# Kernel tuning notes

Hardware: AMD Instinct MI355X
Metric: run time of the kernel (lower is better)

## Reference

```python
import jax, jax.numpy as jnp
import numpy as np

B, S, D_MODEL, N_HEADS, D_K, D_V = 4, 2048, 512, 8, 64, 64
LN_EPS = 1e-5


def setup_inputs() -> dict:
    key = jax.random.key(0)
    ks = jax.random.split(key, 8)
    inp = {
        "input_Q": jax.random.normal(ks[0], (B, S, D_MODEL), dtype=jnp.float32),
        "input_K": jax.random.normal(ks[1], (B, S, D_MODEL), dtype=jnp.float32),
        "input_V": jax.random.normal(ks[2], (B, S, D_MODEL), dtype=jnp.float32),
        "attn_mask": jax.random.randint(ks[3], (B, S, S), 0, 2).astype(jnp.bool_),
        # weights stored [in, out] (torch Linear does x @ W.T; here we use x @ W)
        "W_Q": jax.random.normal(ks[4], (D_MODEL, N_HEADS * D_K), dtype=jnp.float32) * 0.02,
        "W_K": jax.random.normal(ks[5], (D_MODEL, N_HEADS * D_K), dtype=jnp.float32) * 0.02,
        "W_V": jax.random.normal(ks[6], (D_MODEL, N_HEADS * D_V), dtype=jnp.float32) * 0.02,
        "W_O": jax.random.normal(ks[7], (N_HEADS * D_V, D_MODEL), dtype=jnp.float32) * 0.02,
    }
    return inp


def _layernorm(x, eps=LN_EPS):
    mu = jnp.mean(x, axis=-1, keepdims=True)
    var = jnp.mean(jnp.square(x - mu), axis=-1, keepdims=True)
    return (x - mu) * jax.lax.rsqrt(var + eps)


def reference(input_Q, input_K, input_V, attn_mask, W_Q, W_K, W_V, W_O):
    b = input_Q.shape[0]
    # project and split heads: [b, h, s, d]
    Q = (input_Q @ W_Q).reshape(b, -1, N_HEADS, D_K).transpose(0, 2, 1, 3)
    K = (input_K @ W_K).reshape(b, -1, N_HEADS, D_K).transpose(0, 2, 1, 3)
    V = (input_V @ W_V).reshape(b, -1, N_HEADS, D_V).transpose(0, 2, 1, 3)
    scale = 1.0 / np.sqrt(D_K).astype(np.float32)
    # [b, h, s_q, s_k] scores, mask broadcast over heads
    scores = jnp.einsum("bhqd,bhkd->bhqk", Q, K) * scale
    scores = jnp.where(attn_mask[:, None, :, :], jnp.float32(-1e9), scores)
    attn = jax.nn.softmax(scores, axis=-1)
    context = jnp.einsum("bhqk,bhkd->bhqd", attn, V)
    context = context.transpose(0, 2, 1, 3).reshape(b, -1, N_HEADS * D_V)
    output = context @ W_O
    out = _layernorm(output + input_Q)
    return out, attn
```

## Files before the change

kernel.cpp:

```cpp
#include <hip/hip_runtime.h>
#include <hip/hip_bf16.h>
#include <stdint.h>

#define B_  4
#define S_  2048
#define DM  512
#define H_  8
#define DK  64

typedef float        f32x4 __attribute__((ext_vector_type(4)));
typedef short        s16x8 __attribute__((ext_vector_type(8)));
typedef short        s16x4 __attribute__((ext_vector_type(4)));
typedef unsigned int u32x4 __attribute__((ext_vector_type(4)));
typedef unsigned long long u64x4 __attribute__((ext_vector_type(4)));

#define MFMA_B16(a,b,c) __builtin_amdgcn_mfma_f32_16x16x32_bf16(a,b,c,0,0,0)

__device__ __forceinline__ uint32_t bfr(float x) {
  uint32_t u = __float_as_uint(x);
  return (u + 0x7fffu + ((u >> 16) & 1u)) >> 16;
}
__device__ __forceinline__ uint32_t pk2(float a, float b) {
  return ((bfr(b) & 0xffffu) << 16) | (bfr(a) & 0xffffu);
}
__device__ __forceinline__ float uf16(short s) {
  return __uint_as_float(((uint32_t)(uint16_t)s) << 16);
}

__global__ __launch_bounds__(256) void wt_k(const float* __restrict__ w0,
                                            const float* __restrict__ w1,
                                            const float* __restrict__ w2,
                                            const float* __restrict__ w3,
                                            uint16_t* __restrict__ Wt) {
  __shared__ float Ls[64 * 65];
  const int tid = threadIdx.x;
  const int z = blockIdx.z;
  const float* W = (z == 0) ? w0 : (z == 1) ? w1 : (z == 2) ? w2 : w3;
  const int k0 = blockIdx.x * 64, n0 = blockIdx.y * 64;
  {
    const int r = tid >> 2, c = (tid & 3) * 16;
    const float4* src = (const float4*)(W + (size_t)(k0 + r) * 512 + n0 + c);
    float4 v0 = src[0], v1 = src[1], v2 = src[2], v3 = src[3];
    float* d = Ls + r * 65 + c;
    d[0]=v0.x; d[1]=v0.y; d[2]=v0.z;  d[3]=v0.w;
    d[4]=v1.x; d[5]=v1.y; d[6]=v1.z;  d[7]=v1.w;
    d[8]=v2.x; d[9]=v2.y; d[10]=v2.z; d[11]=v2.w;
    d[12]=v3.x;d[13]=v3.y;d[14]=v3.z; d[15]=v3.w;
  }
  __syncthreads();
  uint16_t* dstbase = Wt + (size_t)z * 262144;
#pragma unroll
  for (int i = 0; i < 2; ++i) {
    int nl = i * 32 + (tid >> 3);
    int kc = (tid & 7) * 8;
    s16x8 v;
#pragma unroll
    for (int jj = 0; jj < 8; ++jj) v[jj] = (short)bfr(Ls[(kc + jj) * 65 + nl]);
    *(s16x8*)(dstbase + (size_t)(n0 + nl) * 512 + k0 + kc) = v;
  }
}

__global__ __launch_bounds__(256) void maskpack_k(const int* __restrict__ mask,
                                                  unsigned long long* __restrict__ mbits) {
  const int lane = threadIdx.x & 63;
  const int wid = (blockIdx.x * 256 + threadIdx.x) >> 6;
  for (int w0 = wid * 4; w0 < B_ * S_ * 32; w0 += 8192 * 4) {
    int v0 = __builtin_nontemporal_load(mask + (size_t)(w0 + 0) * 64 + lane);
    int v1 = __builtin_nontemporal_load(mask + (size_t)(w0 + 1) * 64 + lane);
    int v2 = __builtin_nontemporal_load(mask + (size_t)(w0 + 2) * 64 + lane);
    int v3 = __builtin_nontemporal_load(mask + (size_t)(w0 + 3) * 64 + lane);
    unsigned long long b0 = __ballot(v0 != 0), b1 = __ballot(v1 != 0);
    unsigned long long b2 = __ballot(v2 != 0), b3 = __ballot(v3 != 0);
    if (lane == 0) { u64x4 t = {b0, b1, b2, b3}; *(u64x4*)(mbits + w0) = t; }
  }
}

template <bool PROJ>
__global__ __launch_bounds__(256) void gemm2_k(const float* __restrict__ Xq,
                                               const float* __restrict__ Xk,
                                               const float* __restrict__ Xv,
                                               const uint16_t* __restrict__ Wt,
                                               const uint16_t* __restrict__ Actx,
                                               uint16_t* __restrict__ Qkv,
                                               float* __restrict__ Y) {
  __shared__ __hip_bfloat16 As[64 * 64];
  __shared__ __hip_bfloat16 Bs[64 * 64];
  const int tid = threadIdx.x, lane = tid & 63, w = tid >> 6;
  const int l4 = lane >> 4, lc = lane & 15;
  const int p = blockIdx.x;
  const int L = PROJ ? ((p & 7) * 384 + (p >> 3)) : ((p & 7) * 128 + (p >> 3));
  const int yn = L & 7;
  const int xm = PROJ ? ((L >> 3) & 127) : (L >> 3);
  const int z  = PROJ ? (L >> 10) : 3;
  const int m0 = xm * 64, n0 = yn * 64;
  const float* Af = PROJ ? ((z == 0) ? Xq : (z == 1) ? Xk : Xv) : nullptr;
  const uint16_t* Bt = Wt + (size_t)z * 262144;
  const int wm = (w >> 1) * 32, wn = (w & 1) * 32;
  const int ar = tid >> 2, ac = (tid & 3) * 16;
  f32x4 acc[2][2] = {};

  float4 ra[4]; s16x8 rab[2]; s16x8 rb[2];
  auto loadA = [&](int kk) {
    if constexpr (PROJ) {
      const float4* s = (const float4*)(Af + (size_t)(m0 + ar) * 512 + kk + ac);
      ra[0] = s[0]; ra[1] = s[1]; ra[2] = s[2]; ra[3] = s[3];
    } else {
      const uint16_t* s = Actx + (size_t)(m0 + ar) * 512 + kk + ac;
      rab[0] = *(const s16x8*)s; rab[1] = *(const s16x8*)(s + 8);
    }
  };
  auto loadB = [&](int kk) {
    const uint16_t* s = Bt + (size_t)(n0 + ar) * 512 + kk + ac;
    rb[0] = *(const s16x8*)s; rb[1] = *(const s16x8*)(s + 8);
  };
  auto writeAB = [&]() {
    char* da = (char*)As + ar * 128;
    char* db = (char*)Bs + ar * 128;
    const int c0 = (ac * 2) ^ ((ar & 7) << 4);
    const int c1 = (ac * 2 + 16) ^ ((ar & 7) << 4);
    if constexpr (PROJ) {
      u32x4 p0, p1;
      p0.x = pk2(ra[0].x, ra[0].y); p0.y = pk2(ra[0].z, ra[0].w);
      p0.z = pk2(ra[1].x, ra[1].y); p0.w = pk2(ra[1].z, ra[1].w);
      p1.x = pk2(ra[2].x, ra[2].y); p1.y = pk2(ra[2].z, ra[2].w);
      p1.z = pk2(ra[3].x, ra[3].y); p1.w = pk2(ra[3].z, ra[3].w);
      *(u32x4*)(da + c0) = p0; *(u32x4*)(da + c1) = p1;
    } else {
      *(s16x8*)(da + c0) = rab[0]; *(s16x8*)(da + c1) = rab[1];
    }
    *(s16x8*)(db + c0) = rb[0]; *(s16x8*)(db + c1) = rb[1];
  };

  loadA(0); loadB(0); writeAB();
  __syncthreads();
  for (int t = 0; t < 8; ++t) {
    if (t < 7) { loadA((t + 1) * 64); loadB((t + 1) * 64); }
    s16x8 af[2], bg[2];
    __builtin_amdgcn_s_setprio(1);
#pragma unroll
    for (int kf = 0; kf < 2; ++kf) {
#pragma unroll
      for (int mf = 0; mf < 2; ++mf) {
        int row = wm + mf * 16 + lc;
        af[mf] = *(const s16x8*)((char*)As + row * 128 +
                                 ((kf * 64 + l4 * 16) ^ ((row & 7) << 4)));
      }
#pragma unroll
      for (int nf = 0; nf < 2; ++nf) {
        int row = wn + nf * 16 + lc;
        bg[nf] = *(const s16x8*)((char*)Bs + row * 128 +
                                 ((kf * 64 + l4 * 16) ^ ((row & 7) << 4)));
      }
#pragma unroll
      for (int mf = 0; mf < 2; ++mf)
#pragma unroll
        for (int nf = 0; nf < 2; ++nf)
          acc[mf][nf] = MFMA_B16(af[mf], bg[nf], acc[mf][nf]);
    }
    __builtin_amdgcn_s_setprio(0);
    if (t < 7) {
      __syncthreads();
      writeAB();
      __syncthreads();
    }
  }
#pragma unroll
  for (int mf = 0; mf < 2; ++mf)
#pragma unroll
    for (int nf = 0; nf < 2; ++nf) {
      int row = m0 + wm + mf * 16 + l4 * 4;
      int col = n0 + wn + nf * 16 + lc;
#pragma unroll
      for (int j = 0; j < 4; ++j) {
        if constexpr (PROJ)
          (Qkv + (size_t)z * 4194304)[(size_t)(row + j) * 512 + col] =
              (uint16_t)bfr(acc[mf][nf][j]);
        else
          Y[(size_t)(row + j) * 512 + col] = acc[mf][nf][j];
      }
    }
}

__global__ __launch_bounds__(256) void attn_k(const uint16_t* __restrict__ Qb,
                                              const uint16_t* __restrict__ Kb,
                                              const uint16_t* __restrict__ Vb,
                                              const unsigned long long* __restrict__ mbits,
                                              float* __restrict__ attn_out,
                                              uint16_t* __restrict__ ctx) {
  __shared__ __hip_bfloat16 Ks[2][64 * 64];
  __shared__ __hip_bfloat16 Vt[64 * 64];
  __shared__ __hip_bfloat16 Ps[4][16 * 72];
  const int tid = threadIdx.x, lane = tid & 63, w = tid >> 6;
  const int l4 = lane >> 4, lc = lane & 15;
  const int p = blockIdx.x;
  const int L = (p & 7) * 128 + (p >> 3);
  const int qt = L & 31, h = (L >> 5) & 7, b = L >> 8;
  const int qbase = qt * 64;
  const int srow = tid >> 3, scol = tid & 7;

  s16x8 aq0, aq1;
  {
    const uint16_t* qp = Qb + ((size_t)(b * S_ + qbase + w * 16 + lc)) * DM + h * DK + l4 * 8;
    aq0 = *(const s16x8*)qp;
    aq1 = *(const s16x8*)(qp + 32);
  }
  const uint16_t* Kbase = Kb + (size_t)(b * S_) * DM + h * DK;
  const uint16_t* Vbase = Vb + (size_t)(b * S_) * DM + h * DK;
  const unsigned long long* mrow = mbits + ((size_t)(b * S_) + qbase + w * 16 + l4 * 4) * 32;

  float lrun[4] = {0.f, 0.f, 0.f, 0.f};
#pragma unroll
  for (int i = 0; i < 2; ++i) {
    int row = i * 32 + srow;
    s16x8 v = *(const s16x8*)(Kbase + (size_t)row * DM + scol * 8);
    *(s16x8*)((char*)Ks[0] + row * 128 + ((scol * 16) ^ ((row & 7) << 4))) = v;
  }
  __syncthreads();
  for (int kt = 0; kt < 32; ++kt) {
    const int cur = kt & 1;
    const int nxt = (kt < 31) ? kt + 1 : kt;
    s16x8 rk0 = *(const s16x8*)(Kbase + (size_t)(nxt * 64 + srow) * DM + scol * 8);
    s16x8 rk1 = *(const s16x8*)(Kbase + (size_t)(nxt * 64 + 32 + srow) * DM + scol * 8);
    unsigned long long mws[4];
#pragma unroll
    for (int j = 0; j < 4; ++j) mws[j] = mrow[j * 32 + kt];
    f32x4 sacc[4] = {};
    __builtin_amdgcn_s_setprio(1);
#pragma unroll
    for (int nf = 0; nf < 4; ++nf) {
      int row = nf * 16 + lc;
#pragma unroll
      for (int kf = 0; kf < 2; ++kf) {
        s16x8 bk = *(const s16x8*)((char*)Ks[cur] + row * 128 +
                                   ((kf * 64 + l4 * 16) ^ ((row & 7) << 4)));
        sacc[nf] = MFMA_B16(kf ? aq1 : aq0, bk, sacc[nf]);
      }
    }
    __builtin_amdgcn_s_setprio(0);
#pragma unroll
    for (int j = 0; j < 4; ++j)
#pragma unroll
      for (int nf = 0; nf < 4; ++nf) {
        float e = __expf(sacc[nf][j] * 0.125f);
        lrun[j] += ((mws[j] >> (nf * 16 + lc)) & 1ull) ? 0.f : e;
      }
    *(s16x8*)((char*)Ks[cur ^ 1] + srow * 128 + ((scol * 16) ^ ((srow & 7) << 4))) = rk0;
    {
      int row = 32 + srow;
      *(s16x8*)((char*)Ks[cur ^ 1] + row * 128 + ((scol * 16) ^ ((row & 7) << 4))) = rk1;
    }
    __syncthreads();
  }
#pragma unroll
  for (int off = 1; off < 16; off <<= 1)
#pragma unroll
    for (int j = 0; j < 4; ++j) lrun[j] += __shfl_xor(lrun[j], off);
  float Li[4];
#pragma unroll
  for (int j = 0; j < 4; ++j) Li[j] = 1.f / lrun[j];

#pragma unroll
  for (int i = 0; i < 2; ++i) {
    int row = i * 32 + srow;
    s16x8 v = *(const s16x8*)(Kbase + (size_t)row * DM + scol * 8);
    *(s16x8*)((char*)Ks[0] + row * 128 + ((scol * 16) ^ ((row & 7) << 4))) = v;
    s16x8 vv = *(const s16x8*)(Vbase + (size_t)row * DM + scol * 8);
#pragma unroll
    for (int jj = 0; jj < 8; ++jj) {
      int d = scol * 8 + jj;
      *(int16_t*)((char*)Vt + ((d * 128 + row * 2) ^ (scol << 4))) = vv[jj];
    }
  }
  __syncthreads();
  f32x4 cacc[4] = {};
  float* arow = attn_out + (((size_t)(b * H_ + h)) * S_ + qbase + w * 16) * S_;
  for (int kt = 0; kt < 32; ++kt) {
    const int cur = kt & 1;
    const int nxt = (kt < 31) ? kt + 1 : kt;
    s16x8 rk0 = *(const s16x8*)(Kbase + (size_t)(nxt * 64 + srow) * DM + scol * 8);
    s16x8 rk1 = *(const s16x8*)(Kbase + (size_t)(nxt * 64 + 32 + srow) * DM + scol * 8);
    s16x8 rv0 = *(const s16x8*)(Vbase + (size_t)(nxt * 64 + srow) * DM + scol * 8);
    s16x8 rv1 = *(const s16x8*)(Vbase + (size_t)(nxt * 64 + 32 + srow) * DM + scol * 8);
    unsigned long long mws[4];
#pragma unroll
    for (int j = 0; j < 4; ++j) mws[j] = mrow[j * 32 + kt];
    f32x4 sacc[4] = {};
    __builtin_amdgcn_s_setprio(1);
#pragma unroll
    for (int nf = 0; nf < 4; ++nf) {
      int row = nf * 16 + lc;
#pragma unroll
      for (int kf = 0; kf < 2; ++kf) {
        s16x8 bk = *(const s16x8*)((char*)Ks[cur] + row * 128 +
                                   ((kf * 64 + l4 * 16) ^ ((row & 7) << 4)));
        sacc[nf] = MFMA_B16(kf ? aq1 : aq0, bk, sacc[nf]);
      }
    }
    __builtin_amdgcn_s_setprio(0);
#pragma unroll
    for (int j = 0; j < 4; ++j)
#pragma unroll
      for (int nf = 0; nf < 4; ++nf) {
        float e = __expf(sacc[nf][j] * 0.125f);
        float p2 = ((mws[j] >> (nf * 16 + lc)) & 1ull) ? 0.f : e * Li[j];
        *(uint16_t*)((char*)Ps[w] + (l4 * 4 + j) * 144 + (nf * 16 + lc) * 2) = (uint16_t)bfr(p2);
      }
    s16x8 ap0 = *(const s16x8*)((char*)Ps[w] + lc * 144 + l4 * 16);
    s16x8 ap1 = *(const s16x8*)((char*)Ps[w] + lc * 144 + 64 + l4 * 16);
#pragma unroll
    for (int j = 0; j < 4; ++j) {
      const int r = j * 4 + (lane >> 4);
      s16x4 pv = *(const s16x4*)((char*)Ps[w] + r * 144 + (lane & 15) * 8);
      f32x4 o;
      o[0] = uf16(pv[0]); o[1] = uf16(pv[1]); o[2] = uf16(pv[2]); o[3] = uf16(pv[3]);
      __builtin_nontemporal_store(o,
          (f32x4*)(arow + (size_t)r * S_ + kt * 64 + (lane & 15) * 4));
    }
    __builtin_amdgcn_s_setprio(1);
#pragma unroll
    for (int nf = 0; nf < 4; ++nf) {
      int d = nf * 16 + lc;
#pragma unroll
      for (int kf = 0; kf < 2; ++kf) {
        s16x8 bv = *(const s16x8*)((char*)Vt +
                     ((d * 128 + kf * 64 + l4 * 16) ^ ((((d >> 3)) & 7) << 4)));
        cacc[nf] = MFMA_B16(kf ? ap1 : ap0, bv, cacc[nf]);
      }
    }
    __builtin_amdgcn_s_setprio(0);
    __syncthreads();
    *(s16x8*)((char*)Ks[cur ^ 1] + srow * 128 + ((scol * 16) ^ ((srow & 7) << 4))) = rk0;
    {
      int row = 32 + srow;
      *(s16x8*)((char*)Ks[cur ^ 1] + row * 128 + ((scol * 16) ^ ((row & 7) << 4))) = rk1;
    }
#pragma unroll
    for (int jj = 0; jj < 8; ++jj) {
      int d = scol * 8 + jj;
      *(int16_t*)((char*)Vt + ((d * 128 + srow * 2) ^ (scol << 4))) = rv0[jj];
      *(int16_t*)((char*)Vt + ((d * 128 + (32 + srow) * 2) ^ (scol << 4))) = rv1[jj];
    }
    __syncthreads();
  }
#pragma unroll
  for (int nf = 0; nf < 4; ++nf) {
    int d = nf * 16 + lc;
#pragma unroll
    for (int j = 0; j < 4; ++j) {
      int q = qbase + w * 16 + l4 * 4 + j;
      ctx[((size_t)(b * S_ + q)) * DM + h * DK + d] = (uint16_t)bfr(cacc[nf][j]);
    }
  }
}

__global__ __launch_bounds__(256) void ln_k(const float* __restrict__ Y,
                                            const float* __restrict__ X,
                                            float* __restrict__ out) {
  const int lane = threadIdx.x & 63, w = threadIdx.x >> 6;
  const size_t row = (size_t)blockIdx.x * 4 + w;
  const float4* y = (const float4*)(Y + row * 512);
  const float4* x = (const float4*)(X + row * 512);
  float4 a0 = y[lane * 2], a1 = y[lane * 2 + 1];
  float4 b0 = x[lane * 2], b1 = x[lane * 2 + 1];
  float v[8] = {a0.x + b0.x, a0.y + b0.y, a0.z + b0.z, a0.w + b0.w,
                a1.x + b1.x, a1.y + b1.y, a1.z + b1.z, a1.w + b1.w};
  float s = 0.f, ss = 0.f;
#pragma unroll
  for (int j = 0; j < 8; ++j) { s += v[j]; ss += v[j] * v[j]; }
#pragma unroll
  for (int off = 1; off < 64; off <<= 1) {
    s += __shfl_xor(s, off);
    ss += __shfl_xor(ss, off);
  }
  float mean = s * (1.f / 512.f);
  float var = ss * (1.f / 512.f) - mean * mean;
  float rstd = rsqrtf(var + 1e-5f);
  float4 o0 = make_float4((v[0] - mean) * rstd, (v[1] - mean) * rstd,
                          (v[2] - mean) * rstd, (v[3] - mean) * rstd);
  float4 o1 = make_float4((v[4] - mean) * rstd, (v[5] - mean) * rstd,
                          (v[6] - mean) * rstd, (v[7] - mean) * rstd);
  float4* o = (float4*)(out + row * 512);
  o[lane * 2] = o0;
  o[lane * 2 + 1] = o1;
}

extern "C" void kernel_launch(void* const* d_in, const int* in_sizes, int n_in,
                              void* d_out, int out_size, void* d_ws, size_t ws_size,
                              hipStream_t stream) {
  const float* Xq = (const float*)d_in[0];
  const float* Xk = (const float*)d_in[1];
  const float* Xv = (const float*)d_in[2];
  const int*   mask = (const int*)d_in[3];
  const float* Wq = (const float*)d_in[4];
  const float* Wk = (const float*)d_in[5];
  const float* Wv = (const float*)d_in[6];
  const float* Wo = (const float*)d_in[7];

  float* out  = (float*)d_out;
  float* attn = out + (size_t)B_ * S_ * DM;

  char* ws = (char*)d_ws;
  uint16_t* Qb = (uint16_t*)(ws);
  uint16_t* Kb = (uint16_t*)(ws + (8u  << 20));
  uint16_t* Vb = (uint16_t*)(ws + (16u << 20));
  uint16_t* Cx = (uint16_t*)(ws + (24u << 20));
  float*    Y  = (float*)   (ws + (32u << 20));
  uint16_t* Wt = (uint16_t*)(ws + (48u << 20));
  unsigned long long* mb = (unsigned long long*)(ws + (50u << 20));

  wt_k<<<dim3(8, 8, 4), 256, 0, stream>>>(Wq, Wk, Wv, Wo, Wt);
  maskpack_k<<<2048, 256, 0, stream>>>(mask, mb);

  gemm2_k<true><<<3072, 256, 0, stream>>>(Xq, Xk, Xv, Wt, nullptr, Qb, nullptr);

  attn_k<<<1024, 256, 0, stream>>>(Qb, Kb, Vb, mb, attn, Cx);

  gemm2_k<false><<<1024, 256, 0, stream>>>(nullptr, nullptr, nullptr, Wt, Cx, nullptr, Y);
  ln_k<<<2048, 256, 0, stream>>>(Y, Xq, out);
}
```

Baseline: 238.5 us.

## Enlarge GEMM tiles to 128x128 and merge weight-transpose with mask packing

The projection and output GEMMs now use 128x128 block tiles, with each wave computing a 64x64 sub-tile (4x4 MFMA fragments) instead of 32x32. This raises data reuse per LDS load and cuts redundant global reads of the activations and weights. The price is more registers and fewer blocks: 768 and 256, which gives low occupancy on 256 CUs for the output GEMM. The weight transpose/convert and mask bit-packing kernels are also merged into one launch to save a kernel launch.

New measurement: 226.6 us. 1.05x faster.

```diff
diff --git a/kernel.cpp b/kernel.cpp
--- a/kernel.cpp
+++ b/kernel.cpp
@@ -27,134 +27,146 @@
   return __uint_as_float(((uint32_t)(uint16_t)s) << 16);
 }
 
-__global__ __launch_bounds__(256) void wt_k(const float* __restrict__ w0,
-                                            const float* __restrict__ w1,
-                                            const float* __restrict__ w2,
-                                            const float* __restrict__ w3,
-                                            uint16_t* __restrict__ Wt) {
+__global__ __launch_bounds__(256) void prep_k(const float* __restrict__ w0,
+                                              const float* __restrict__ w1,
+                                              const float* __restrict__ w2,
+                                              const float* __restrict__ w3,
+                                              uint16_t* __restrict__ Wt,
+                                              const int* __restrict__ mask,
+                                              unsigned long long* __restrict__ mbits) {
   __shared__ float Ls[64 * 65];
   const int tid = threadIdx.x;
-  const int z = blockIdx.z;
-  const float* W = (z == 0) ? w0 : (z == 1) ? w1 : (z == 2) ? w2 : w3;
-  const int k0 = blockIdx.x * 64, n0 = blockIdx.y * 64;
-  {
-    const int r = tid >> 2, c = (tid & 3) * 16;
-    const float4* src = (const float4*)(W + (size_t)(k0 + r) * 512 + n0 + c);
-    float4 v0 = src[0], v1 = src[1], v2 = src[2], v3 = src[3];
-    float* d = Ls + r * 65 + c;
-    d[0]=v0.x; d[1]=v0.y; d[2]=v0.z;  d[3]=v0.w;
-    d[4]=v1.x; d[5]=v1.y; d[6]=v1.z;  d[7]=v1.w;
-    d[8]=v2.x; d[9]=v2.y; d[10]=v2.z; d[11]=v2.w;
-    d[12]=v3.x;d[13]=v3.y;d[14]=v3.z; d[15]=v3.w;
-  }
-  __syncthreads();
-  uint16_t* dstbase = Wt + (size_t)z * 262144;
-#pragma unroll
-  for (int i = 0; i < 2; ++i) {
-    int nl = i * 32 + (tid >> 3);
-    int kc = (tid & 7) * 8;
-    s16x8 v;
-#pragma unroll
-    for (int jj = 0; jj < 8; ++jj) v[jj] = (short)bfr(Ls[(kc + jj) * 65 + nl]);
-    *(s16x8*)(dstbase + (size_t)(n0 + nl) * 512 + k0 + kc) = v;
-  }
-}
-
-__global__ __launch_bounds__(256) void maskpack_k(const int* __restrict__ mask,
-                                                  unsigned long long* __restrict__ mbits) {
-  const int lane = threadIdx.x & 63;
-  const int wid = (blockIdx.x * 256 + threadIdx.x) >> 6;
-  for (int w0 = wid * 4; w0 < B_ * S_ * 32; w0 += 8192 * 4) {
-    int v0 = __builtin_nontemporal_load(mask + (size_t)(w0 + 0) * 64 + lane);
-    int v1 = __builtin_nontemporal_load(mask + (size_t)(w0 + 1) * 64 + lane);
-    int v2 = __builtin_nontemporal_load(mask + (size_t)(w0 + 2) * 64 + lane);
-    int v3 = __builtin_nontemporal_load(mask + (size_t)(w0 + 3) * 64 + lane);
-    unsigned long long b0 = __ballot(v0 != 0), b1 = __ballot(v1 != 0);
-    unsigned long long b2 = __ballot(v2 != 0), b3 = __ballot(v3 != 0);
-    if (lane == 0) { u64x4 t = {b0, b1, b2, b3}; *(u64x4*)(mbits + w0) = t; }
+  if (blockIdx.x < 256) {
+    const int bx = blockIdx.x;
+    const int z = bx >> 6;
+    const int k0 = ((bx >> 3) & 7) * 64, n0 = (bx & 7) * 64;
+    const float* W = (z == 0) ? w0 : (z == 1) ? w1 : (z == 2) ? w2 : w3;
+    {
+      const int r = tid >> 2, c = (tid & 3) * 16;
+      const float4* src = (const float4*)(W + (size_t)(k0 + r) * 512 + n0 + c);
+      float4 v0 = src[0], v1 = src[1], v2 = src[2], v3 = src[3];
+      float* d = Ls + r * 65 + c;
+      d[0]=v0.x; d[1]=v0.y; d[2]=v0.z;  d[3]=v0.w;
+      d[4]=v1.x; d[5]=v1.y; d[6]=v1.z;  d[7]=v1.w;
+      d[8]=v2.x; d[9]=v2.y; d[10]=v2.z; d[11]=v2.w;
+      d[12]=v3.x;d[13]=v3.y;d[14]=v3.z; d[15]=v3.w;
+    }
+    __syncthreads();
+    uint16_t* dstbase = Wt + (size_t)z * 262144;
+#pragma unroll
+    for (int i = 0; i < 2; ++i) {
+      int nl = i * 32 + (tid >> 3);
+      int kc = (tid & 7) * 8;
+      s16x8 v;
+#pragma unroll
+      for (int jj = 0; jj < 8; ++jj) v[jj] = (short)bfr(Ls[(kc + jj) * 65 + nl]);
+      *(s16x8*)(dstbase + (size_t)(n0 + nl) * 512 + k0 + kc) = v;
+    }
+  } else {
+    const int lane = tid & 63;
+    const int wid = ((blockIdx.x - 256) * 256 + tid) >> 6;
+    for (int w0i = wid * 4; w0i < B_ * S_ * 32; w0i += 8192 * 4) {
+      int v0 = __builtin_nontemporal_load(mask + (size_t)(w0i + 0) * 64 + lane);
+      int v1 = __builtin_nontemporal_load(mask + (size_t)(w0i + 1) * 64 + lane);
+      int v2 = __builtin_nontemporal_load(mask + (size_t)(w0i + 2) * 64 + lane);
+      int v3 = __builtin_nontemporal_load(mask + (size_t)(w0i + 3) * 64 + lane);
+      unsigned long long b0 = __ballot(v0 != 0), b1 = __ballot(v1 != 0);
+      unsigned long long b2 = __ballot(v2 != 0), b3 = __ballot(v3 != 0);
+      if (lane == 0) { u64x4 t = {b0, b1, b2, b3}; *(u64x4*)(mbits + w0i) = t; }
+    }
   }
 }
 
 template <bool PROJ>
-__global__ __launch_bounds__(256) void gemm2_k(const float* __restrict__ Xq,
+__global__ __launch_bounds__(256) void gemm3_k(const float* __restrict__ Xq,
                                                const float* __restrict__ Xk,
                                                const float* __restrict__ Xv,
                                                const uint16_t* __restrict__ Wt,
                                                const uint16_t* __restrict__ Actx,
                                                uint16_t* __restrict__ Qkv,
                                                float* __restrict__ Y) {
-  __shared__ __hip_bfloat16 As[64 * 64];
-  __shared__ __hip_bfloat16 Bs[64 * 64];
+  __shared__ __hip_bfloat16 As[128 * 64];
+  __shared__ __hip_bfloat16 Bs[128 * 64];
   const int tid = threadIdx.x, lane = tid & 63, w = tid >> 6;
   const int l4 = lane >> 4, lc = lane & 15;
   const int p = blockIdx.x;
-  const int L = PROJ ? ((p & 7) * 384 + (p >> 3)) : ((p & 7) * 128 + (p >> 3));
-  const int yn = L & 7;
-  const int xm = PROJ ? ((L >> 3) & 127) : (L >> 3);
-  const int z  = PROJ ? (L >> 10) : 3;
-  const int m0 = xm * 64, n0 = yn * 64;
+  int xm, yn, z;
+  if constexpr (PROJ) {
+    const int L = (p & 7) * 96 + (p >> 3);
+    z = L >> 8; const int r = L & 255; xm = r >> 2; yn = r & 3;
+  } else {
+    const int L = (p & 7) * 32 + (p >> 3);
+    z = 3; xm = L >> 2; yn = L & 3;
+  }
+  const int m0 = xm * 128, n0 = yn * 128;
   const float* Af = PROJ ? ((z == 0) ? Xq : (z == 1) ? Xk : Xv) : nullptr;
   const uint16_t* Bt = Wt + (size_t)z * 262144;
-  const int wm = (w >> 1) * 32, wn = (w & 1) * 32;
-  const int ar = tid >> 2, ac = (tid & 3) * 16;
-  f32x4 acc[2][2] = {};
-
-  float4 ra[4]; s16x8 rab[2]; s16x8 rb[2];
+  const int wm = (w >> 1) * 64, wn = (w & 1) * 64;
+  const int srow = tid >> 3;
+  const int scol = tid & 7;
+  f32x4 acc[4][4] = {};
+
+  float4 raA[4], raB[4]; s16x8 rab[4]; s16x8 rb[4];
   auto loadA = [&](int kk) {
-    if constexpr (PROJ) {
-      const float4* s = (const float4*)(Af + (size_t)(m0 + ar) * 512 + kk + ac);
-      ra[0] = s[0]; ra[1] = s[1]; ra[2] = s[2]; ra[3] = s[3];
-    } else {
-      const uint16_t* s = Actx + (size_t)(m0 + ar) * 512 + kk + ac;
-      rab[0] = *(const s16x8*)s; rab[1] = *(const s16x8*)(s + 8);
+#pragma unroll
+    for (int i = 0; i < 4; ++i) {
+      int row = i * 32 + srow;
+      if constexpr (PROJ) {
+        const float4* s = (const float4*)(Af + (size_t)(m0 + row) * 512 + kk + scol * 8);
+        raA[i] = s[0]; raB[i] = s[1];
+      } else {
+        rab[i] = *(const s16x8*)(Actx + (size_t)(m0 + row) * 512 + kk + scol * 8);
+      }
     }
   };
   auto loadB = [&](int kk) {
-    const uint16_t* s = Bt + (size_t)(n0 + ar) * 512 + kk + ac;
-    rb[0] = *(const s16x8*)s; rb[1] = *(const s16x8*)(s + 8);
+#pragma unroll
+    for (int i = 0; i < 4; ++i) {
+      int row = i * 32 + srow;
+      rb[i] = *(const s16x8*)(Bt + (size_t)(n0 + row) * 512 + kk + scol * 8);
+    }
   };
   auto writeAB = [&]() {
-    char* da = (char*)As + ar * 128;
-    char* db = (char*)Bs + ar * 128;
-    const int c0 = (ac * 2) ^ ((ar & 7) << 4);
-    const int c1 = (ac * 2 + 16) ^ ((ar & 7) << 4);
-    if constexpr (PROJ) {
-      u32x4 p0, p1;
-      p0.x = pk2(ra[0].x, ra[0].y); p0.y = pk2(ra[0].z, ra[0].w);
-      p0.z = pk2(ra[1].x, ra[1].y); p0.w = pk2(ra[1].z, ra[1].w);
-      p1.x = pk2(ra[2].x, ra[2].y); p1.y = pk2(ra[2].z, ra[2].w);
-      p1.z = pk2(ra[3].x, ra[3].y); p1.w = pk2(ra[3].z, ra[3].w);
-      *(u32x4*)(da + c0) = p0; *(u32x4*)(da + c1) = p1;
-    } else {
-      *(s16x8*)(da + c0) = rab[0]; *(s16x8*)(da + c1) = rab[1];
-    }
-    *(s16x8*)(db + c0) = rb[0]; *(s16x8*)(db + c1) = rb[1];
+#pragma unroll
+    for (int i = 0; i < 4; ++i) {
+      int row = i * 32 + srow;
+      const int c = (scol * 16) ^ ((row & 7) << 4);
+      if constexpr (PROJ) {
+        u32x4 v;
+        v.x = pk2(raA[i].x, raA[i].y); v.y = pk2(raA[i].z, raA[i].w);
+        v.z = pk2(raB[i].x, raB[i].y); v.w = pk2(raB[i].z, raB[i].w);
+        *(u32x4*)((char*)As + row * 128 + c) = v;
+      } else {
+        *(s16x8*)((char*)As + row * 128 + c) = rab[i];
+      }
+      *(s16x8*)((char*)Bs + row * 128 + c) = rb[i];
+    }
   };
 
   loadA(0); loadB(0); writeAB();
   __syncthreads();
   for (int t = 0; t < 8; ++t) {
     if (t < 7) { loadA((t + 1) * 64); loadB((t + 1) * 64); }
-    s16x8 af[2], bg[2];
     __builtin_amdgcn_s_setprio(1);
 #pragma unroll
     for (int kf = 0; kf < 2; ++kf) {
-#pragma unroll
-      for (int mf = 0; mf < 2; ++mf) {
+      s16x8 af[4], bg[4];
+#pragma unroll
+      for (int mf = 0; mf < 4; ++mf) {
         int row = wm + mf * 16 + lc;
         af[mf] = *(const s16x8*)((char*)As + row * 128 +
                                  ((kf * 64 + l4 * 16) ^ ((row & 7) << 4)));
       }
 #pragma unroll
-      for (int nf = 0; nf < 2; ++nf) {
+      for (int nf = 0; nf < 4; ++nf) {
         int row = wn + nf * 16 + lc;
         bg[nf] = *(const s16x8*)((char*)Bs + row * 128 +
                                  ((kf * 64 + l4 * 16) ^ ((row & 7) << 4)));
       }
 #pragma unroll
-      for (int mf = 0; mf < 2; ++mf)
-#pragma unroll
-        for (int nf = 0; nf < 2; ++nf)
+      for (int mf = 0; mf < 4; ++mf)
+#pragma unroll
+        for (int nf = 0; nf < 4; ++nf)
           acc[mf][nf] = MFMA_B16(af[mf], bg[nf], acc[mf][nf]);
     }
     __builtin_amdgcn_s_setprio(0);
@@ -165,9 +177,9 @@
     }
   }
 #pragma unroll
-  for (int mf = 0; mf < 2; ++mf)
-#pragma unroll
-    for (int nf = 0; nf < 2; ++nf) {
+  for (int mf = 0; mf < 4; ++mf)
+#pragma unroll
+    for (int nf = 0; nf < 4; ++nf) {
       int row = m0 + wm + mf * 16 + l4 * 4;
       int col = n0 + wn + nf * 16 + lc;
 #pragma unroll
@@ -408,13 +420,12 @@
   uint16_t* Wt = (uint16_t*)(ws + (48u << 20));
   unsigned long long* mb = (unsigned long long*)(ws + (50u << 20));
 
-  wt_k<<<dim3(8, 8, 4), 256, 0, stream>>>(Wq, Wk, Wv, Wo, Wt);
-  maskpack_k<<<2048, 256, 0, stream>>>(mask, mb);
-
-  gemm2_k<true><<<3072, 256, 0, stream>>>(Xq, Xk, Xv, Wt, nullptr, Qb, nullptr);
+  prep_k<<<2304, 256, 0, stream>>>(Wq, Wk, Wv, Wo, Wt, mask, mb);
+
+  gemm3_k<true><<<768, 256, 0, stream>>>(Xq, Xk, Xv, Wt, nullptr, Qb, nullptr);
 
   attn_k<<<1024, 256, 0, stream>>>(Qb, Kb, Vb, mb, attn, Cx);
 
-  gemm2_k<false><<<1024, 256, 0, stream>>>(nullptr, nullptr, nullptr, Wt, Cx, nullptr, Y);
+  gemm3_k<false><<<256, 256, 0, stream>>>(nullptr, nullptr, nullptr, Wt, Cx, nullptr, Y);
   ln_k<<<2048, 256, 0, stream>>>(Y, Xq, out);
 }
```
